# Kernel tuning notes

Hardware: AMD Instinct MI355X
Metric: run time of the kernel (lower is better)

Reference implementation:

```python
import jax, jax.numpy as jnp
import numpy as np

BN_EPS = 1e-5


def setup_inputs() -> dict:
    key = jax.random.key(0)
    ks = jax.random.split(key, 12)
    B, T, S = 8, 256, 64
    D = 256  # 2*u, u=128
    sc = lambda fan: 1.0 / np.sqrt(fan)
    return {
        "Hx": jax.random.normal(ks[0], (B, T, D), dtype=jnp.float32),
        "Hs": jax.random.normal(ks[1], (S, D), dtype=jnp.float32),
        # transformS = BatchNorm1d(D) -> Linear(D,D) -> ReLU -> Linear(D,D)
        "bn_gamma": jnp.ones((D,), jnp.float32),
        "bn_beta": jnp.zeros((D,), jnp.float32),
        "s_w1": jax.random.normal(ks[2], (D, D), jnp.float32) * sc(D),
        "s_b1": jnp.zeros((D,), jnp.float32),
        "s_w2": jax.random.normal(ks[3], (D, D), jnp.float32) * sc(D),
        "s_b2": jnp.zeros((D,), jnp.float32),
        # W = Linear(3D, D) -> ReLU -> Linear(D, 1)   (6u = 3D features)
        "w_w1": jax.random.normal(ks[4], (3 * D, D), jnp.float32) * sc(3 * D),
        "w_b1": jnp.zeros((D,), jnp.float32),
        "w_w2": jax.random.normal(ks[5], (D, 1), jnp.float32) * sc(D),
        "w_b2": jnp.zeros((1,), jnp.float32),
        "truthSeqY": jax.random.randint(ks[6], (B, T, S), 0, 2, dtype=jnp.int32),
        "inputLen": jax.random.randint(ks[7], (B,), 1, T, dtype=jnp.int32),
    }


def reference(Hx, Hs, bn_gamma, bn_beta, s_w1, s_b1, s_w2, s_b2,
              w_w1, w_b1, w_w2, w_b2, truthSeqY, inputLen):
    B, T, D = Hx.shape
    S = Hs.shape[0]

    # transformS: BatchNorm1d (training-mode batch stats over slot dim) + 2-layer MLP
    mu = jnp.mean(Hs, axis=0)
    var = jnp.var(Hs, axis=0)  # biased, as torch BN uses for normalization
    hs = (Hs - mu) * jax.lax.rsqrt(var + BN_EPS) * bn_gamma + bn_beta
    transHs = jax.nn.relu(hs @ s_w1 + s_b1) @ s_w2 + s_b2  # [S, D]

    # pairwise broadcast: cat(Hx, transHs, Hx*transHs) over [B,T,S,3D]
    mx = jnp.broadcast_to(Hx[:, :, None, :], (B, T, S, D))
    ms = jnp.broadcast_to(transHs[None, None, :, :], (B, T, S, D))
    feat = jnp.concatenate([mx, ms, mx * ms], axis=-1)  # [B,T,S,3D]

    # scoring MLP -> scalar per (token, slot)
    h = jax.nn.relu(feat @ w_w1 + w_b1)        # [B,T,S,D]
    atten = (h @ w_w2 + w_b2)[..., 0]          # [B,T,S]

    atten_score = jax.nn.softmax(atten, axis=2)             # softmax over slots
    G = jnp.einsum('bts,sd->btd', atten_score, transHs)     # weighted slot agg
    outputU = jnp.concatenate([Hx, G + Hx], axis=2)         # [B,T,2D]
    return outputU, atten_score
```

## Files before the change

kernel.cpp:

```cpp
#include <hip/hip_runtime.h>
#include <math.h>

#define DD 256
#define SS 64
#define BT 2048

typedef __attribute__((ext_vector_type(4))) float f32x4;
typedef __attribute__((ext_vector_type(8))) short bf16x8;
typedef __attribute__((ext_vector_type(4))) unsigned int u32x4;

typedef __attribute__((address_space(3))) unsigned lds_u32;
typedef const __attribute__((address_space(1))) unsigned glb_u32;

__device__ inline unsigned pack_bf16(float a, float b) {
    unsigned ua = __builtin_bit_cast(unsigned, a);
    unsigned ub = __builtin_bit_cast(unsigned, b);
    ua = (ua + 0x7fffu + ((ua >> 16) & 1u)) >> 16;
    ub = (ub + 0x7fffu + ((ub >> 16) & 1u)) >> 16;
    return ua | (ub << 16);
}

__global__ __launch_bounds__(1024) void
k_prep2(const float* __restrict__ Hs, const float* __restrict__ g,
        const float* __restrict__ b, const float* __restrict__ s_w1,
        const float* __restrict__ s_b1, const float* __restrict__ s_w2,
        const float* __restrict__ s_b2, const float* __restrict__ w_w1,
        const float* __restrict__ w_b1, float* __restrict__ transHs,
        float* __restrict__ S1b) {
    __shared__ float rowA[DD], rowB[DD], rowC[DD];
    __shared__ float red[8][DD];
    const int s = blockIdx.x;
    const int j = threadIdx.x & 255, kw = threadIdx.x >> 8;
    float sum = 0.f, sumsq = 0.f;
#pragma unroll
    for (int s2 = kw * 16; s2 < kw * 16 + 16; ++s2) {
        float v = Hs[s2 * DD + j];
        sum += v; sumsq += v * v;
    }
    red[kw][j] = sum; red[4 + kw][j] = sumsq;
    __syncthreads();
    if (kw == 0) {
        float st = red[0][j] + red[1][j] + red[2][j] + red[3][j];
        float sq = red[4][j] + red[5][j] + red[6][j] + red[7][j];
        float mu  = st * (1.f / SS);
        float var = sq * (1.f / SS) - mu * mu;
        rowA[j] = (Hs[s * DD + j] - mu) * rsqrtf(var + 1e-5f) * g[j] + b[j];
    }
    __syncthreads();
    float a1 = 0.f;
#pragma unroll 16
    for (int d = kw * 64; d < kw * 64 + 64; ++d)
        a1 = fmaf(rowA[d], s_w1[d * DD + j], a1);
    red[kw][j] = a1;
    __syncthreads();
    if (kw == 0)
        rowB[j] = fmaxf(red[0][j] + red[1][j] + red[2][j] + red[3][j] + s_b1[j], 0.f);
    __syncthreads();
    float a2 = 0.f;
#pragma unroll 16
    for (int d = kw * 64; d < kw * 64 + 64; ++d)
        a2 = fmaf(rowB[d], s_w2[d * DD + j], a2);
    red[kw][j] = a2;
    __syncthreads();
    if (kw == 0) {
        float r = red[0][j] + red[1][j] + red[2][j] + red[3][j] + s_b2[j];
        rowC[j] = r;
        transHs[s * DD + j] = r;
    }
    __syncthreads();
    float a3 = 0.f;
#pragma unroll 16
    for (int d = kw * 64; d < kw * 64 + 64; ++d)
        a3 = fmaf(rowC[d], w_w1[(256 + d) * DD + j], a3);
    red[kw][j] = a3;
    __syncthreads();
    if (kw == 0)
        S1b[s * DD + j] = red[0][j] + red[1][j] + red[2][j] + red[3][j] + w_b1[j];
}

__global__ __launch_bounds__(256) void
k_pack_a(const float* __restrict__ Hx, unsigned* __restrict__ Apack) {
    int idx = blockIdx.x * 256 + threadIdx.x;
    int lane = idx & 63, ks = (idx >> 6) & 7, MT = idx >> 9;
    int t  = MT * 16 + (lane & 15);
    int k0 = ks * 32 + (lane >> 4) * 8;
    const float* src = Hx + t * DD + k0;
    float4 x0 = *(const float4*)src;
    float4 x1 = *(const float4*)(src + 4);
    unsigned p[4];
    p[0] = pack_bf16(x0.x, x0.y);
    p[1] = pack_bf16(x0.z, x0.w);
    p[2] = pack_bf16(x1.x, x1.y);
    p[3] = pack_bf16(x1.z, x1.w);
    *(u32x4*)(Apack + idx * 4) = *(const u32x4*)p;
}

__global__ __launch_bounds__(256) void
k_pack_bs(const float* __restrict__ w_w1, const float* __restrict__ transHs,
          unsigned* __restrict__ Bs) {
    __shared__ float ms_l[16][DD];
    const int ic = blockIdx.x & 31, sg = blockIdx.x >> 5;
    const int s0 = sg * 16;
    const int tid = threadIdx.x;
#pragma unroll
    for (int i = 0; i < 4; ++i) {
        int e4 = i * 256 + tid;
        ((float4*)ms_l)[e4] = ((const float4*)(transHs + s0 * DD))[e4];
    }
    __syncthreads();
    const int idx = ic * 256 + tid;
    const int lane = idx & 63, ks = (idx >> 6) & 7, nt = idx >> 9;
    const int j  = nt * 16 + (lane & 15);
    const int k0 = ks * 32 + (lane >> 4) * 8;
    const float* C   = w_w1 + 512 * DD;
    float w1v[8], cv[8];
#pragma unroll
    for (int e = 0; e < 8; ++e) {
        w1v[e] = w_w1[(k0 + e) * DD + j];
        cv[e]  = C[(k0 + e) * DD + j];
    }
    for (int ss = 0; ss < 16; ++ss) {
        unsigned p[4];
#pragma unroll
        for (int e = 0; e < 4; ++e) {
            float f0 = w1v[2 * e]     + ms_l[ss][k0 + 2 * e]     * cv[2 * e];
            float f1 = w1v[2 * e + 1] + ms_l[ss][k0 + 2 * e + 1] * cv[2 * e + 1];
            p[e] = pack_bf16(f0, f1);
        }
        *(u32x4*)(Bs + ((s0 + ss) * 8192 + idx) * 4) = *(const u32x4*)p;
    }
}

__global__ __launch_bounds__(256, 2) void
k_main_mfma(const unsigned* __restrict__ Apack, const unsigned* __restrict__ Bs,
            const float* __restrict__ S1b, const float* __restrict__ w2,
            const float* __restrict__ w_b2, float* __restrict__ atten) {
    __shared__ unsigned Albs[16384];
    const int swz  = (blockIdx.x & 7) * 128 + (blockIdx.x >> 3);
    const int s    = swz >> 4;
    const int tile = swz & 15;
    const int t0 = tile * 128;
    const int tid = threadIdx.x;
    const int w = tid >> 6, l = tid & 63;
    const int lrow = l & 15, lg = l >> 4;
    const unsigned* Asrc = Apack + tile * 16384;
    const unsigned* Bsl  = Bs + s * 32768;

#pragma unroll
    for (int i = 0; i < 16; ++i) {
        int chunk = w * 16 + i;
        __builtin_amdgcn_global_load_lds((glb_u32*)(Asrc + chunk * 256 + l * 4),
                                         (lds_u32*)(Albs + chunk * 256), 16, 0, 0);
    }
    __syncthreads();

    f32x4 acc[8][4] = {};
#pragma unroll
    for (int ks = 0; ks < 8; ++ks) {
        bf16x8 af[8];
#pragma unroll
        for (int mt = 0; mt < 8; ++mt)
            af[mt] = *(const bf16x8*)((const char*)Albs + ((mt * 8 + ks) * 64 + l) * 16);
#pragma unroll
        for (int nt = 0; nt < 4; ++nt) {
            const bf16x8 bf = *(const bf16x8*)(Bsl + (((w * 4 + nt) * 8 + ks) * 64 + l) * 4);
#pragma unroll
            for (int mt = 0; mt < 8; ++mt)
                acc[mt][nt] = __builtin_amdgcn_mfma_f32_16x16x32_bf16(af[mt], bf, acc[mt][nt], 0, 0, 0);
        }
    }
    __syncthreads();

    float* attp = (float*)Albs;
    float s1[4], w2v[4];
#pragma unroll
    for (int nt = 0; nt < 4; ++nt) {
        int jn = (w * 4 + nt) * 16 + lrow;
        s1[nt]  = S1b[s * DD + jn];
        w2v[nt] = w2[jn];
    }
#pragma unroll
    for (int mt = 0; mt < 8; ++mt) {
#pragma unroll
        for (int i = 0; i < 4; ++i) {
            float p = 0.f;
#pragma unroll
            for (int nt = 0; nt < 4; ++nt) {
                float h = fmaxf(acc[mt][nt][i] + s1[nt], 0.f);
                p = fmaf(h, w2v[nt], p);
            }
            p += __shfl_xor(p, 1);
            p += __shfl_xor(p, 2);
            p += __shfl_xor(p, 4);
            p += __shfl_xor(p, 8);
            if (lrow == 0) attp[w * 128 + mt * 16 + lg * 4 + i] = p;
        }
    }
    __syncthreads();
    if (tid < 128) {
        float r = attp[tid] + attp[128 + tid] + attp[256 + tid] + attp[384 + tid] + w_b2[0];
        atten[(t0 + tid) * SS + s] = r;
    }
}

__global__ __launch_bounds__(256) void
k_out(const float* __restrict__ Hx, const float* __restrict__ m,
      const float* __restrict__ atten, float* __restrict__ outU,
      float* __restrict__ outA) {
    int wave = threadIdx.x >> 6, lane = threadIdx.x & 63;
    int t = blockIdx.x * 4 + wave;
    float a = atten[t * SS + lane];
    float mx = a;
#pragma unroll
    for (int off = 32; off; off >>= 1) mx = fmaxf(mx, __shfl_xor(mx, off));
    float e = __expf(a - mx);
    float sum = e;
#pragma unroll
    for (int off = 32; off; off >>= 1) sum += __shfl_xor(sum, off);
    float p = e / sum;
    outA[t * SS + lane] = p;
    float gacc[4] = {};
    for (int s = 0; s < SS; ++s) {
        float ps = __shfl(p, s);
#pragma unroll
        for (int q = 0; q < 4; ++q)
            gacc[q] = fmaf(ps, m[s * DD + lane + 64 * q], gacc[q]);
    }
#pragma unroll
    for (int q = 0; q < 4; ++q) {
        int j = lane + 64 * q;
        float x = Hx[t * DD + j];
        outU[t * 2 * DD + j] = x;
        outU[t * 2 * DD + DD + j] = x + gacc[q];
    }
}

extern "C" void kernel_launch(void* const* d_in, const int* in_sizes, int n_in,
                              void* d_out, int out_size, void* d_ws, size_t ws_size,
                              hipStream_t stream) {
    const float* Hx   = (const float*)d_in[0];
    const float* Hs   = (const float*)d_in[1];
    const float* bn_g = (const float*)d_in[2];
    const float* bn_b = (const float*)d_in[3];
    const float* s_w1 = (const float*)d_in[4];
    const float* s_b1 = (const float*)d_in[5];
    const float* s_w2 = (const float*)d_in[6];
    const float* s_b2 = (const float*)d_in[7];
    const float* w_w1 = (const float*)d_in[8];
    const float* w_b1 = (const float*)d_in[9];
    const float* w_w2 = (const float*)d_in[10];
    const float* w_b2 = (const float*)d_in[11];

    float* ws      = (float*)d_ws;
    float* transHs = ws;
    float* S1b     = ws + 16384;
    float* atten   = ws + 32768;
    unsigned* Apack = (unsigned*)(ws + 163840);
    unsigned* Bs    = Apack + 262144;

    float* outU = (float*)d_out;
    float* outA = outU + BT * 2 * DD;

    k_prep2<<<SS, 1024, 0, stream>>>(Hs, bn_g, bn_b, s_w1, s_b1, s_w2, s_b2,
                                     w_w1, w_b1, transHs, S1b);
    k_pack_a<<<256, 256, 0, stream>>>(Hx, Apack);
    k_pack_bs<<<128, 256, 0, stream>>>(w_w1, transHs, Bs);
    k_main_mfma<<<1024, 256, 0, stream>>>(Apack, Bs, S1b, w_w2, w_b2, atten);
    k_out<<<BT / 4, 256, 0, stream>>>(Hx, transHs, atten, outU, outA);
}
```

Baseline: 61.26 us.

## Merge pack kernels and reuse A tile across two slots with 512-thread blocks

The two packing kernels are merged into one launch, with blocks split by index between packing A and packing B, which removes one kernel launch. The main MFMA kernel now uses 512 threads (8 waves, 2 N-tiles each) and loops over two slots per block, so the A tile loaded into LDS is reused for both slots and the grid halves. Block-to-slot mapping is grouped per XCD. This trades more serial work per block and extra barriers for less LDS refill traffic and fewer launches.

```diff
diff --git a/kernel.cpp b/kernel.cpp
--- a/kernel.cpp
+++ b/kernel.cpp
@@ -79,127 +79,127 @@
 }
 
 __global__ __launch_bounds__(256) void
-k_pack_a(const float* __restrict__ Hx, unsigned* __restrict__ Apack) {
-    int idx = blockIdx.x * 256 + threadIdx.x;
-    int lane = idx & 63, ks = (idx >> 6) & 7, MT = idx >> 9;
-    int t  = MT * 16 + (lane & 15);
-    int k0 = ks * 32 + (lane >> 4) * 8;
-    const float* src = Hx + t * DD + k0;
-    float4 x0 = *(const float4*)src;
-    float4 x1 = *(const float4*)(src + 4);
-    unsigned p[4];
-    p[0] = pack_bf16(x0.x, x0.y);
-    p[1] = pack_bf16(x0.z, x0.w);
-    p[2] = pack_bf16(x1.x, x1.y);
-    p[3] = pack_bf16(x1.z, x1.w);
-    *(u32x4*)(Apack + idx * 4) = *(const u32x4*)p;
-}
-
-__global__ __launch_bounds__(256) void
-k_pack_bs(const float* __restrict__ w_w1, const float* __restrict__ transHs,
-          unsigned* __restrict__ Bs) {
-    __shared__ float ms_l[16][DD];
-    const int ic = blockIdx.x & 31, sg = blockIdx.x >> 5;
-    const int s0 = sg * 16;
+k_pack(const float* __restrict__ Hx, const float* __restrict__ w_w1,
+       const float* __restrict__ transHs, unsigned* __restrict__ Apack,
+       unsigned* __restrict__ Bs) {
+    const int bid = blockIdx.x;
     const int tid = threadIdx.x;
-#pragma unroll
-    for (int i = 0; i < 4; ++i) {
-        int e4 = i * 256 + tid;
-        ((float4*)ms_l)[e4] = ((const float4*)(transHs + s0 * DD))[e4];
-    }
-    __syncthreads();
-    const int idx = ic * 256 + tid;
-    const int lane = idx & 63, ks = (idx >> 6) & 7, nt = idx >> 9;
-    const int j  = nt * 16 + (lane & 15);
-    const int k0 = ks * 32 + (lane >> 4) * 8;
-    const float* C   = w_w1 + 512 * DD;
-    float w1v[8], cv[8];
-#pragma unroll
-    for (int e = 0; e < 8; ++e) {
-        w1v[e] = w_w1[(k0 + e) * DD + j];
-        cv[e]  = C[(k0 + e) * DD + j];
-    }
-    for (int ss = 0; ss < 16; ++ss) {
+    if (bid < 256) {
+        int idx = bid * 256 + tid;
+        int lane = idx & 63, ks = (idx >> 6) & 7, MT = idx >> 9;
+        int t  = MT * 16 + (lane & 15);
+        int k0 = ks * 32 + (lane >> 4) * 8;
+        const float* src = Hx + t * DD + k0;
+        float4 x0 = *(const float4*)src;
+        float4 x1 = *(const float4*)(src + 4);
         unsigned p[4];
-#pragma unroll
-        for (int e = 0; e < 4; ++e) {
-            float f0 = w1v[2 * e]     + ms_l[ss][k0 + 2 * e]     * cv[2 * e];
-            float f1 = w1v[2 * e + 1] + ms_l[ss][k0 + 2 * e + 1] * cv[2 * e + 1];
-            p[e] = pack_bf16(f0, f1);
-        }
-        *(u32x4*)(Bs + ((s0 + ss) * 8192 + idx) * 4) = *(const u32x4*)p;
-    }
-}
-
-__global__ __launch_bounds__(256, 2) void
+        p[0] = pack_bf16(x0.x, x0.y);
+        p[1] = pack_bf16(x0.z, x0.w);
+        p[2] = pack_bf16(x1.x, x1.y);
+        p[3] = pack_bf16(x1.z, x1.w);
+        *(u32x4*)(Apack + idx * 4) = *(const u32x4*)p;
+    } else {
+        __shared__ float ms_l[16][DD];
+        const int b2 = bid - 256;
+        const int ic = b2 & 31, sg = b2 >> 5;
+        const int s0 = sg * 16;
+#pragma unroll
+        for (int i = 0; i < 4; ++i) {
+            int e4 = i * 256 + tid;
+            ((float4*)ms_l)[e4] = ((const float4*)(transHs + s0 * DD))[e4];
+        }
+        __syncthreads();
+        const int idx = ic * 256 + tid;
+        const int lane = idx & 63, ks = (idx >> 6) & 7, nt = idx >> 9;
+        const int j  = nt * 16 + (lane & 15);
+        const int k0 = ks * 32 + (lane >> 4) * 8;
+        const float* C = w_w1 + 512 * DD;
+        float w1v[8], cv[8];
+#pragma unroll
+        for (int e = 0; e < 8; ++e) {
+            w1v[e] = w_w1[(k0 + e) * DD + j];
+            cv[e]  = C[(k0 + e) * DD + j];
+        }
+        for (int ss = 0; ss < 16; ++ss) {
+            unsigned p[4];
+#pragma unroll
+            for (int e = 0; e < 4; ++e) {
+                float f0 = w1v[2 * e]     + ms_l[ss][k0 + 2 * e]     * cv[2 * e];
+                float f1 = w1v[2 * e + 1] + ms_l[ss][k0 + 2 * e + 1] * cv[2 * e + 1];
+                p[e] = pack_bf16(f0, f1);
+            }
+            *(u32x4*)(Bs + ((s0 + ss) * 8192 + idx) * 4) = *(const u32x4*)p;
+        }
+    }
+}
+
+__global__ __launch_bounds__(512, 4) void
 k_main_mfma(const unsigned* __restrict__ Apack, const unsigned* __restrict__ Bs,
             const float* __restrict__ S1b, const float* __restrict__ w2,
             const float* __restrict__ w_b2, float* __restrict__ atten) {
     __shared__ unsigned Albs[16384];
-    const int swz  = (blockIdx.x & 7) * 128 + (blockIdx.x >> 3);
-    const int s    = swz >> 4;
-    const int tile = swz & 15;
+    __shared__ float attp[8][128];
+    const int bid = blockIdx.x;
+    const int xcd = bid & 7, li = bid >> 3;
+    const int sp  = xcd * 4 + (li >> 4);
+    const int tile = li & 15;
     const int t0 = tile * 128;
     const int tid = threadIdx.x;
     const int w = tid >> 6, l = tid & 63;
     const int lrow = l & 15, lg = l >> 4;
     const unsigned* Asrc = Apack + tile * 16384;
-    const unsigned* Bsl  = Bs + s * 32768;
-
-#pragma unroll
-    for (int i = 0; i < 16; ++i) {
-        int chunk = w * 16 + i;
+
+#pragma unroll
+    for (int i = 0; i < 8; ++i) {
+        int chunk = w * 8 + i;
         __builtin_amdgcn_global_load_lds((glb_u32*)(Asrc + chunk * 256 + l * 4),
                                          (lds_u32*)(Albs + chunk * 256), 16, 0, 0);
     }
     __syncthreads();
 
-    f32x4 acc[8][4] = {};
-#pragma unroll
-    for (int ks = 0; ks < 8; ++ks) {
-        bf16x8 af[8];
-#pragma unroll
-        for (int mt = 0; mt < 8; ++mt)
-            af[mt] = *(const bf16x8*)((const char*)Albs + ((mt * 8 + ks) * 64 + l) * 16);
-#pragma unroll
-        for (int nt = 0; nt < 4; ++nt) {
-            const bf16x8 bf = *(const bf16x8*)(Bsl + (((w * 4 + nt) * 8 + ks) * 64 + l) * 4);
+    const float w2v0 = w2[(w * 2 + 0) * 16 + lrow];
+    const float w2v1 = w2[(w * 2 + 1) * 16 + lrow];
+
+    for (int sl = 0; sl < 2; ++sl) {
+        const int s = sp * 2 + sl;
+        const unsigned* Bsl = Bs + s * 32768;
+        f32x4 acc[8][2] = {};
+#pragma unroll
+        for (int ks = 0; ks < 8; ++ks) {
+            bf16x8 af[8];
 #pragma unroll
             for (int mt = 0; mt < 8; ++mt)
-                acc[mt][nt] = __builtin_amdgcn_mfma_f32_16x16x32_bf16(af[mt], bf, acc[mt][nt], 0, 0, 0);
-        }
-    }
-    __syncthreads();
-
-    float* attp = (float*)Albs;
-    float s1[4], w2v[4];
-#pragma unroll
-    for (int nt = 0; nt < 4; ++nt) {
-        int jn = (w * 4 + nt) * 16 + lrow;
-        s1[nt]  = S1b[s * DD + jn];
-        w2v[nt] = w2[jn];
-    }
-#pragma unroll
-    for (int mt = 0; mt < 8; ++mt) {
-#pragma unroll
-        for (int i = 0; i < 4; ++i) {
-            float p = 0.f;
-#pragma unroll
-            for (int nt = 0; nt < 4; ++nt) {
-                float h = fmaxf(acc[mt][nt][i] + s1[nt], 0.f);
-                p = fmaf(h, w2v[nt], p);
+                af[mt] = *(const bf16x8*)((const char*)Albs + ((mt * 8 + ks) * 64 + l) * 16);
+#pragma unroll
+            for (int nt = 0; nt < 2; ++nt) {
+                const bf16x8 bf = *(const bf16x8*)(Bsl + (((w * 2 + nt) * 8 + ks) * 64 + l) * 4);
+#pragma unroll
+                for (int mt = 0; mt < 8; ++mt)
+                    acc[mt][nt] = __builtin_amdgcn_mfma_f32_16x16x32_bf16(af[mt], bf, acc[mt][nt], 0, 0, 0);
             }
-            p += __shfl_xor(p, 1);
-            p += __shfl_xor(p, 2);
-            p += __shfl_xor(p, 4);
-            p += __shfl_xor(p, 8);
-            if (lrow == 0) attp[w * 128 + mt * 16 + lg * 4 + i] = p;
-        }
-    }
-    __syncthreads();
-    if (tid < 128) {
-        float r = attp[tid] + attp[128 + tid] + attp[256 + tid] + attp[384 + tid] + w_b2[0];
-        atten[(t0 + tid) * SS + s] = r;
+        }
+        const float s10 = S1b[s * DD + (w * 2 + 0) * 16 + lrow];
+        const float s11 = S1b[s * DD + (w * 2 + 1) * 16 + lrow];
+#pragma unroll
+        for (int mt = 0; mt < 8; ++mt) {
+#pragma unroll
+            for (int i = 0; i < 4; ++i) {
+                float p = fmaxf(acc[mt][0][i] + s10, 0.f) * w2v0
+                        + fmaxf(acc[mt][1][i] + s11, 0.f) * w2v1;
+                p += __shfl_xor(p, 1);
+                p += __shfl_xor(p, 2);
+                p += __shfl_xor(p, 4);
+                p += __shfl_xor(p, 8);
+                if (lrow == 0) attp[w][mt * 16 + lg * 4 + i] = p;
+            }
+        }
+        __syncthreads();
+        if (tid < 128) {
+            float r = attp[0][tid] + attp[1][tid] + attp[2][tid] + attp[3][tid]
+                    + attp[4][tid] + attp[5][tid] + attp[6][tid] + attp[7][tid] + w_b2[0];
+            atten[(t0 + tid) * SS + s] = r;
+        }
+        __syncthreads();
     }
 }
 
@@ -263,8 +263,7 @@
 
     k_prep2<<<SS, 1024, 0, stream>>>(Hs, bn_g, bn_b, s_w1, s_b1, s_w2, s_b2,
                                      w_w1, w_b1, transHs, S1b);
-    k_pack_a<<<256, 256, 0, stream>>>(Hx, Apack);
-    k_pack_bs<<<128, 256, 0, stream>>>(w_w1, transHs, Bs);
-    k_main_mfma<<<1024, 256, 0, stream>>>(Apack, Bs, S1b, w_w2, w_b2, atten);
+    k_pack<<<384, 256, 0, stream>>>(Hx, w_w1, transHs, Apack, Bs);
+    k_main_mfma<<<512, 512, 0, stream>>>(Apack, Bs, S1b, w_w2, w_b2, atten);
     k_out<<<BT / 4, 256, 0, stream>>>(Hx, transHs, atten, outU, outA);
 }
```

Result: slower. 63.57 us (+3.8%).
